# Kernel tuning notes

Measured on AMD Instinct MI355X. Metric: run time of the kernel, lower is better.

The kernel has to match this reference:

```python
import jax, jax.numpy as jnp
import numpy as np

NEG_BIG = -9.0e15  # matches -9000000000000000.0 fill in the torch code


def setup_inputs() -> dict:
    key = jax.random.key(0)
    ks = jax.random.split(key, 8)
    N, Fin, Fout = 8192, 256, 128
    input = jax.random.normal(ks[0], (N, Fin), dtype=jnp.float32)
    adj = jax.random.randint(ks[1], (N, N), 0, 2, dtype=jnp.int32)
    s_fc = 1.0 / np.sqrt(Fin)
    s_at = 1.0 / np.sqrt(Fout)
    W_fc = jax.random.normal(ks[2], (Fin, Fout), dtype=jnp.float32) * s_fc
    b_fc = jax.random.normal(ks[3], (Fout,), dtype=jnp.float32) * s_fc
    w_ax = jax.random.normal(ks[4], (Fout, 1), dtype=jnp.float32) * s_at
    b_ax = jax.random.normal(ks[5], (1,), dtype=jnp.float32) * s_at
    w_an = jax.random.normal(ks[6], (Fout, 1), dtype=jnp.float32) * s_at
    b_an = jax.random.normal(ks[7], (1,), dtype=jnp.float32) * s_at
    return {"input": input, "adj": adj, "W_fc": W_fc, "b_fc": b_fc,
            "w_ax": w_ax, "b_ax": b_ax, "w_an": w_an, "b_an": b_an}


def reference(input, adj, W_fc, b_fc, w_ax, b_ax, w_an, b_an):
    # x = fc(input): [N, Fout]
    x = input @ W_fc + b_fc
    # rank-1 additive scores: att_x(x) [N,1] + att_nei(x).T [1,N] -> [N,N]
    x_att = x @ w_ax + b_ax          # [N, 1]
    neib_att = (x @ w_an + b_an).T   # [1, N]
    ws = x_att + neib_att            # [N, N]
    # adjacency mask + row softmax
    ws = jnp.where(adj > 0, ws, NEG_BIG)
    ws = jax.nn.softmax(ws, axis=1)
    # dense aggregation + residual + ELU (dropout is identity in eval)
    out = jax.nn.elu(x + ws @ x)
    return out
```

## Files before the change

### kernel.cpp

```cpp
#include <hip/hip_runtime.h>
#include <hip/hip_bf16.h>
#include <math.h>


using f32x4  = __attribute__((ext_vector_type(4))) float;
using bf16x8 = __attribute__((ext_vector_type(8))) short;

#define N_NODES 8192
#define FIN     256
#define FOUT    128
#define NPAD    144
#define NSPLIT  8
#define KCHUNK  (N_NODES / NSPLIT)

#define X_OFF    0u
#define T_OFF    (X_OFF + N_NODES*FOUT*4u)
#define PMAX_OFF (T_OFF + N_NODES*4u)
#define GMAX_OFF (PMAX_OFF + 512u)
#define YT_OFF   (GMAX_OFF + 512u)
#define P_OFF    (YT_OFF + (size_t)NPAD*N_NODES*2u)

__device__ __forceinline__ unsigned short f2bf(float f) {
  unsigned int u = __float_as_uint(f);
  unsigned int r = (u + 0x7FFFu + ((u >> 16) & 1u)) >> 16;
  return (unsigned short)r;
}

__global__ __launch_bounds__(256) void k1_fc(const float* __restrict__ in,
    const float* __restrict__ Wfc, const float* __restrict__ bfc,
    float* __restrict__ x) {
  __shared__ float sm[16 * FIN];
  const int tid = threadIdx.x;
  const int r0  = blockIdx.x * 16;
  const float4* gin = reinterpret_cast<const float4*>(in + (size_t)r0 * FIN);
  float4* sm4 = reinterpret_cast<float4*>(sm);
  #pragma unroll
  for (int i = 0; i < 4; i++) sm4[i * 256 + tid] = gin[i * 256 + tid];
  __syncthreads();
  const int d = tid & 127, g = tid >> 7;
  const float bias = bfc[d];
  float acc[8];
  #pragma unroll
  for (int r = 0; r < 8; r++) acc[r] = bias;
  const float4* s4 = reinterpret_cast<const float4*>(sm);
  for (int k = 0; k < FIN; k += 4) {
    float w0 = Wfc[(k + 0) * FOUT + d];
    float w1 = Wfc[(k + 1) * FOUT + d];
    float w2 = Wfc[(k + 2) * FOUT + d];
    float w3 = Wfc[(k + 3) * FOUT + d];
    #pragma unroll
    for (int r = 0; r < 8; r++) {
      float4 iv = s4[((g * 8 + r) * FIN + k) >> 2];
      acc[r] = fmaf(iv.x, w0, acc[r]);
      acc[r] = fmaf(iv.y, w1, acc[r]);
      acc[r] = fmaf(iv.z, w2, acc[r]);
      acc[r] = fmaf(iv.w, w3, acc[r]);
    }
  }
  #pragma unroll
  for (int r = 0; r < 8; r++)
    x[(size_t)(r0 + g * 8 + r) * FOUT + d] = acc[r];
}

__global__ __launch_bounds__(256) void k2_att(const float* __restrict__ x,
    const float* __restrict__ wan, const float* __restrict__ ban,
    float* __restrict__ t, float* __restrict__ pmax) {
  __shared__ float wm[4];
  const int tid = threadIdx.x, lane = tid & 63, w = tid >> 6;
  const float w0 = wan[lane], w1 = wan[lane + 64];
  const float bb = ban[0];
  float tmax = -1e30f;
  const int rbase = blockIdx.x * 128 + w * 32;
  for (int rr = 0; rr < 32; rr++) {
    const int row = rbase + rr;
    float p = x[(size_t)row * FOUT + lane] * w0
            + x[(size_t)row * FOUT + 64 + lane] * w1;
    #pragma unroll
    for (int m = 1; m < 64; m <<= 1) p += __shfl_xor(p, m);
    const float tv = p + bb;
    if (lane == 0) t[row] = tv;
    tmax = fmaxf(tmax, tv);
  }
  if (lane == 0) wm[w] = tmax;
  __syncthreads();
  if (tid == 0)
    pmax[blockIdx.x] = fmaxf(fmaxf(wm[0], wm[1]), fmaxf(wm[2], wm[3]));
}

__global__ void k3_gmax(const float* __restrict__ pmax, float* __restrict__ gmax) {
  float v = pmax[threadIdx.x];
  #pragma unroll
  for (int m = 1; m < 64; m <<= 1) v = fmaxf(v, __shfl_xor(v, m));
  if (threadIdx.x == 0) gmax[0] = v;
}

__global__ __launch_bounds__(256) void k4_y(const float* __restrict__ x,
    const float* __restrict__ t, const float* __restrict__ gmax,
    unsigned short* __restrict__ Yt) {
  const int tid = threadIdx.x, lane = tid & 63, w = tid >> 6;
  const int j = blockIdx.x * 64 + lane;
  const float e = expf(t[j] - gmax[0]);
  const float4* x4 = reinterpret_cast<const float4*>(x + (size_t)j * FOUT + w * 32);
  #pragma unroll
  for (int dd = 0; dd < 8; dd++) {
    float4 xv = x4[dd];
    const int d = w * 32 + dd * 4;
    Yt[(size_t)(d + 0) * N_NODES + j] = f2bf(e * xv.x);
    Yt[(size_t)(d + 1) * N_NODES + j] = f2bf(e * xv.y);
    Yt[(size_t)(d + 2) * N_NODES + j] = f2bf(e * xv.z);
    Yt[(size_t)(d + 3) * N_NODES + j] = f2bf(e * xv.w);
  }
  if (w == 0) {
    Yt[(size_t)128 * N_NODES + j] = f2bf(e);
    #pragma unroll
    for (int r = 129; r < NPAD; r++) Yt[(size_t)r * N_NODES + j] = 0;
  }
}

__global__ __launch_bounds__(256) void k5_gemm(const int* __restrict__ adj,
    const unsigned short* __restrict__ Yt, float* __restrict__ P) {
  const int tid  = threadIdx.x;
  const int lane = tid & 63, w = tid >> 6;
  const int bm = blockIdx.x, s = blockIdx.y;
  const int q  = lane >> 4;
  const int arow = bm * 64 + w * 16 + (lane & 15);
  const int* aptr = adj + (size_t)arow * N_NODES + s * KCHUNK + q * 8;
  const unsigned short* bbase =
      Yt + (size_t)(lane & 15) * N_NODES + s * KCHUNK + q * 8;

  f32x4 acc[9];
  #pragma unroll
  for (int nf = 0; nf < 9; nf++) acc[nf] = (f32x4){0.f, 0.f, 0.f, 0.f};

  for (int k = 0; k < KCHUNK; k += 32) {
    int4 a0 = *reinterpret_cast<const int4*>(aptr + k);
    int4 a1 = *reinterpret_cast<const int4*>(aptr + k + 4);
    union { bf16x8 v; unsigned int u[4]; } af;
    af.u[0] = (unsigned int)(a0.x | (a0.y << 16)) * 0x3F80u;
    af.u[1] = (unsigned int)(a0.z | (a0.w << 16)) * 0x3F80u;
    af.u[2] = (unsigned int)(a1.x | (a1.y << 16)) * 0x3F80u;
    af.u[3] = (unsigned int)(a1.z | (a1.w << 16)) * 0x3F80u;
    bf16x8 bf[9];
    #pragma unroll
    for (int nf = 0; nf < 9; nf++)
      bf[nf] = *reinterpret_cast<const bf16x8*>(bbase + (size_t)nf * 16 * N_NODES + k);
    #pragma unroll
    for (int nf = 0; nf < 9; nf++)
      acc[nf] = __builtin_amdgcn_mfma_f32_16x16x32_bf16(af.v, bf[nf], acc[nf], 0, 0, 0);
  }

  float* Pp = P + (size_t)s * N_NODES * NPAD;
  const int colb = lane & 15;
  #pragma unroll
  for (int nf = 0; nf < 9; nf++) {
    if (nf == 8 && colb != 0) continue;
    #pragma unroll
    for (int r = 0; r < 4; r++) {
      const int grow = bm * 64 + w * 16 + q * 4 + r;
      Pp[(size_t)grow * NPAD + nf * 16 + colb] = acc[nf][r];
    }
  }
}

__global__ __launch_bounds__(256) void k6_fin(const float* __restrict__ P,
    const float* __restrict__ x, float* __restrict__ out) {
  const int gid = blockIdx.x * 256 + threadIdx.x;
  const int i = gid >> 7, d = gid & 127;
  const size_t base = (size_t)i * NPAD;
  float num = 0.f, Z = 0.f;
  #pragma unroll
  for (int s = 0; s < NSPLIT; s++) {
    num += P[(size_t)s * N_NODES * NPAD + base + d];
    Z   += P[(size_t)s * N_NODES * NPAD + base + 128];
  }
  const float agg = (Z > 0.f) ? num / Z : 0.f;
  const float v = x[(size_t)i * FOUT + d] + agg;
  out[gid] = (v > 0.f) ? v : expm1f(v);
}

extern "C" void kernel_launch(void* const* d_in, const int* in_sizes, int n_in,
                              void* d_out, int out_size, void* d_ws, size_t ws_size,
                              hipStream_t stream) {
  const float* input = (const float*)d_in[0];
  const int*   adj   = (const int*)d_in[1];
  const float* Wfc   = (const float*)d_in[2];
  const float* bfc   = (const float*)d_in[3];
  const float* wan   = (const float*)d_in[6];
  const float* ban   = (const float*)d_in[7];

  char* ws = (char*)d_ws;
  float*          x    = (float*)(ws + X_OFF);
  float*          t    = (float*)(ws + T_OFF);
  float*          pmax = (float*)(ws + PMAX_OFF);
  float*          gmax = (float*)(ws + GMAX_OFF);
  unsigned short* Yt   = (unsigned short*)(ws + YT_OFF);
  float*          P    = (float*)(ws + P_OFF);
  float*          out  = (float*)d_out;

  k1_fc  <<<dim3(512),        dim3(256), 0, stream>>>(input, Wfc, bfc, x);
  k2_att <<<dim3(64),         dim3(256), 0, stream>>>(x, wan, ban, t, pmax);
  k3_gmax<<<dim3(1),          dim3(64),  0, stream>>>(pmax, gmax);
  k4_y   <<<dim3(128),        dim3(256), 0, stream>>>(x, t, gmax, Yt);
  k5_gemm<<<dim3(128, NSPLIT),dim3(256), 0, stream>>>(adj, Yt, P);
  k6_fin <<<dim3(4096),       dim3(256), 0, stream>>>(P, x, out);
}
```

Baseline: 537.7 us.

## Pre-swizzle Y into MFMA fragment layout and software-pipeline adjacency loads

```diff
diff --git a/kernel.cpp b/kernel.cpp
--- a/kernel.cpp
+++ b/kernel.cpp
@@ -16,7 +16,7 @@
 #define X_OFF    0u
 #define T_OFF    (X_OFF + N_NODES*FOUT*4u)
 #define PMAX_OFF (T_OFF + N_NODES*4u)
-#define GMAX_OFF (PMAX_OFF + 512u)
+#define GMAX_OFF (PMAX_OFF + 1024u)
 #define YT_OFF   (GMAX_OFF + 512u)
 #define P_OFF    (YT_OFF + (size_t)NPAD*N_NODES*2u)
 
@@ -70,8 +70,8 @@
   const float w0 = wan[lane], w1 = wan[lane + 64];
   const float bb = ban[0];
   float tmax = -1e30f;
-  const int rbase = blockIdx.x * 128 + w * 32;
-  for (int rr = 0; rr < 32; rr++) {
+  const int rbase = blockIdx.x * 32 + w * 8;
+  for (int rr = 0; rr < 8; rr++) {
     const int row = rbase + rr;
     float p = x[(size_t)row * FOUT + lane] * w0
             + x[(size_t)row * FOUT + 64 + lane] * w1;
@@ -88,7 +88,8 @@
 }
 
 __global__ void k3_gmax(const float* __restrict__ pmax, float* __restrict__ gmax) {
-  float v = pmax[threadIdx.x];
+  float v = fmaxf(fmaxf(pmax[threadIdx.x], pmax[threadIdx.x + 64]),
+                  fmaxf(pmax[threadIdx.x + 128], pmax[threadIdx.x + 192]));
   #pragma unroll
   for (int m = 1; m < 64; m <<= 1) v = fmaxf(v, __shfl_xor(v, m));
   if (threadIdx.x == 0) gmax[0] = v;
@@ -96,58 +97,84 @@
 
 __global__ __launch_bounds__(256) void k4_y(const float* __restrict__ x,
     const float* __restrict__ t, const float* __restrict__ gmax,
-    unsigned short* __restrict__ Yt) {
+    unsigned short* __restrict__ Yf) {
+  __shared__ unsigned short sm[NPAD * 64];
   const int tid = threadIdx.x, lane = tid & 63, w = tid >> 6;
-  const int j = blockIdx.x * 64 + lane;
+  const int jj = lane, j = blockIdx.x * 64 + jj;
   const float e = expf(t[j] - gmax[0]);
   const float4* x4 = reinterpret_cast<const float4*>(x + (size_t)j * FOUT + w * 32);
   #pragma unroll
   for (int dd = 0; dd < 8; dd++) {
     float4 xv = x4[dd];
-    const int d = w * 32 + dd * 4;
-    Yt[(size_t)(d + 0) * N_NODES + j] = f2bf(e * xv.x);
-    Yt[(size_t)(d + 1) * N_NODES + j] = f2bf(e * xv.y);
-    Yt[(size_t)(d + 2) * N_NODES + j] = f2bf(e * xv.z);
-    Yt[(size_t)(d + 3) * N_NODES + j] = f2bf(e * xv.w);
-  }
-  if (w == 0) {
-    Yt[(size_t)128 * N_NODES + j] = f2bf(e);
-    #pragma unroll
-    for (int r = 129; r < NPAD; r++) Yt[(size_t)r * N_NODES + j] = 0;
+    const int c = w * 32 + dd * 4;
+    sm[(c + 0) * 64 + jj] = f2bf(e * xv.x);
+    sm[(c + 1) * 64 + jj] = f2bf(e * xv.y);
+    sm[(c + 2) * 64 + jj] = f2bf(e * xv.z);
+    sm[(c + 3) * 64 + jj] = f2bf(e * xv.w);
+  }
+  #pragma unroll
+  for (int i = 0; i < 4; i++) {
+    const int c = 128 + w * 4 + i;
+    sm[c * 64 + jj] = (c == 128) ? f2bf(e) : (unsigned short)0;
+  }
+  __syncthreads();
+  for (int c5 = w; c5 < 18; c5 += 4) {
+    const int wnd = c5 / 9, nf = c5 % 9;
+    const int srcIdx = (nf * 16 + (lane & 15)) * 64 + wnd * 32 + (lane >> 4) * 8;
+    bf16x8 v = *reinterpret_cast<const bf16x8*>(&sm[srcIdx]);
+    const size_t Wg = (size_t)blockIdx.x * 2 + wnd;
+    *reinterpret_cast<bf16x8*>(Yf + (Wg * 9 + nf) * 512 + lane * 8) = v;
   }
 }
 
 __global__ __launch_bounds__(256) void k5_gemm(const int* __restrict__ adj,
-    const unsigned short* __restrict__ Yt, float* __restrict__ P) {
+    const unsigned short* __restrict__ Yf, float* __restrict__ P) {
   const int tid  = threadIdx.x;
   const int lane = tid & 63, w = tid >> 6;
   const int bm = blockIdx.x, s = blockIdx.y;
   const int q  = lane >> 4;
   const int arow = bm * 64 + w * 16 + (lane & 15);
   const int* aptr = adj + (size_t)arow * N_NODES + s * KCHUNK + q * 8;
-  const unsigned short* bbase =
-      Yt + (size_t)(lane & 15) * N_NODES + s * KCHUNK + q * 8;
+  const unsigned short* bptr = Yf + ((size_t)s * (KCHUNK / 32) * 9) * 512 + lane * 8;
 
   f32x4 acc[9];
   #pragma unroll
   for (int nf = 0; nf < 9; nf++) acc[nf] = (f32x4){0.f, 0.f, 0.f, 0.f};
 
-  for (int k = 0; k < KCHUNK; k += 32) {
-    int4 a0 = *reinterpret_cast<const int4*>(aptr + k);
-    int4 a1 = *reinterpret_cast<const int4*>(aptr + k + 4);
-    union { bf16x8 v; unsigned int u[4]; } af;
-    af.u[0] = (unsigned int)(a0.x | (a0.y << 16)) * 0x3F80u;
-    af.u[1] = (unsigned int)(a0.z | (a0.w << 16)) * 0x3F80u;
-    af.u[2] = (unsigned int)(a1.x | (a1.y << 16)) * 0x3F80u;
-    af.u[3] = (unsigned int)(a1.z | (a1.w << 16)) * 0x3F80u;
-    bf16x8 bf[9];
-    #pragma unroll
-    for (int nf = 0; nf < 9; nf++)
-      bf[nf] = *reinterpret_cast<const bf16x8*>(bbase + (size_t)nf * 16 * N_NODES + k);
-    #pragma unroll
-    for (int nf = 0; nf < 9; nf++)
-      acc[nf] = __builtin_amdgcn_mfma_f32_16x16x32_bf16(af.v, bf[nf], acc[nf], 0, 0, 0);
-  }
+#define LOAD_A(dst0, dst1, kk_) \
+    dst0 = *reinterpret_cast<const int4*>(aptr + (kk_)); \
+    dst1 = *reinterpret_cast<const int4*>(aptr + (kk_) + 4);
+
+#define CONV_MFMA(a0_, a1_, kk_) { \
+    bf16x8 bf[9]; \
+    const unsigned short* bw = bptr + (size_t)((kk_) >> 5) * 9 * 512; \
+    _Pragma("unroll") \
+    for (int nf = 0; nf < 9; nf++) \
+      bf[nf] = *reinterpret_cast<const bf16x8*>(bw + nf * 512); \
+    union { bf16x8 v; unsigned int u[4]; } af; \
+    af.u[0] = (unsigned int)((a0_).x | ((a0_).y << 16)) * 0x3F80u; \
+    af.u[1] = (unsigned int)((a0_).z | ((a0_).w << 16)) * 0x3F80u; \
+    af.u[2] = (unsigned int)((a1_).x | ((a1_).y << 16)) * 0x3F80u; \
+    af.u[3] = (unsigned int)((a1_).z | ((a1_).w << 16)) * 0x3F80u; \
+    _Pragma("unroll") \
+    for (int nf = 0; nf < 9; nf++) \
+      acc[nf] = __builtin_amdgcn_mfma_f32_16x16x32_bf16(af.v, bf[nf], acc[nf], 0, 0, 0); \
+  }
+
+  int4 A0a, A0b, A1a, A1b, A2a, A2b, A3a, A3b;
+  LOAD_A(A0a, A0b, 0);
+  LOAD_A(A1a, A1b, 32);
+  for (int kk = 0; kk <= KCHUNK - 128; kk += 64) {
+    LOAD_A(A2a, A2b, kk + 64);
+    CONV_MFMA(A0a, A0b, kk);
+    LOAD_A(A3a, A3b, kk + 96);
+    CONV_MFMA(A1a, A1b, kk + 32);
+    A0a = A2a; A0b = A2b; A1a = A3a; A1b = A3b;
+  }
+  CONV_MFMA(A0a, A0b, KCHUNK - 64);
+  CONV_MFMA(A1a, A1b, KCHUNK - 32);
+#undef LOAD_A
+#undef CONV_MFMA
 
   float* Pp = P + (size_t)s * N_NODES * NPAD;
   const int colb = lane & 15;
@@ -193,14 +220,14 @@
   float*          t    = (float*)(ws + T_OFF);
   float*          pmax = (float*)(ws + PMAX_OFF);
   float*          gmax = (float*)(ws + GMAX_OFF);
-  unsigned short* Yt   = (unsigned short*)(ws + YT_OFF);
+  unsigned short* Yf   = (unsigned short*)(ws + YT_OFF);
   float*          P    = (float*)(ws + P_OFF);
   float*          out  = (float*)d_out;
 
-  k1_fc  <<<dim3(512),        dim3(256), 0, stream>>>(input, Wfc, bfc, x);
-  k2_att <<<dim3(64),         dim3(256), 0, stream>>>(x, wan, ban, t, pmax);
-  k3_gmax<<<dim3(1),          dim3(64),  0, stream>>>(pmax, gmax);
-  k4_y   <<<dim3(128),        dim3(256), 0, stream>>>(x, t, gmax, Yt);
-  k5_gemm<<<dim3(128, NSPLIT),dim3(256), 0, stream>>>(adj, Yt, P);
-  k6_fin <<<dim3(4096),       dim3(256), 0, stream>>>(P, x, out);
-}
+  k1_fc  <<<dim3(512),         dim3(256), 0, stream>>>(input, Wfc, bfc, x);
+  k2_att <<<dim3(256),         dim3(256), 0, stream>>>(x, wan, ban, t, pmax);
+  k3_gmax<<<dim3(1),           dim3(64),  0, stream>>>(pmax, gmax);
+  k4_y   <<<dim3(128),         dim3(256), 0, stream>>>(x, t, gmax, Yf);
+  k5_gemm<<<dim3(128, NSPLIT), dim3(256), 0, stream>>>(adj, Yf, P);
+  k6_fin <<<dim3(4096),        dim3(256), 0, stream>>>(P, x, out);
+}
```

Measured after the change: 482.0 us. 10.4% less time.
